# Optimization experiments

Measured on AMD Instinct MI355X. Metric: run time of the kernel, lower is better.

The kernel has to match this reference:

```python
import jax, jax.numpy as jnp
import numpy as np

WINDOW = 1024
UNITS = 128


def setup_inputs() -> dict:
    key = jax.random.key(0)
    k1, k2, k3 = jax.random.split(key, 3)
    input_tensor = jax.random.normal(k1, (1, UNITS), dtype=jnp.float32)
    state = jax.random.normal(k2, (UNITS, WINDOW), dtype=jnp.float32)
    w = jax.random.normal(k3, (2 * UNITS + 1, UNITS), dtype=jnp.float32) * 0.05
    b = jnp.zeros((UNITS,), dtype=jnp.float32)
    return {"input_tensor": input_tensor, "state": state, "w": w, "b": b}


def reference(input_tensor, state, w, b):
    U, W = state.shape
    # state @ state_shift (shift matrix with ones on subdiagonal) == drop first column
    shifted_state = state[:, 1:]                          # [U, W-1]
    new_state = jnp.concatenate([shifted_state, input_tensor.T], axis=-1)  # [U, W]
    fs = new_state.T                                      # flip_state: [W, U]

    # h_i[i,j,:] = fs[j];  h_j[i,j,:] = fs[i]
    # se_ij = concat([h_i, h_j, <h_i,h_j>], -1); sim = se_ij @ w + b
    # Split w so we never materialize the [W,W,2U+1] concat tensor:
    w_hi = w[:U]        # [U, U] multiplies h_i (fs[j])
    w_hj = w[U:2 * U]   # [U, U] multiplies h_j (fs[i])
    w_dot = w[2 * U]    # [U]    multiplies the pairwise dot product

    proj_hi = fs @ w_hi                                   # [W, U], indexed by j
    proj_hj = fs @ w_hj                                   # [W, U], indexed by i
    d = fs @ fs.T                                         # [W, W] pairwise dots

    # sim[i,j,u] = proj_hi[j,u] + proj_hj[i,u] + d[i,j]*w_dot[u] + b[u]
    sim = proj_hi[None, :, :] + proj_hj[:, None, :] + d[:, :, None] * w_dot + b  # [W,W,U]
    a = jax.nn.softmax(sim, axis=1)                       # softmax over j

    # c[i,u] = sum_j h_i[i,j,u] * a[i,j,u] = sum_j fs[j,u] * a[i,j,u]
    c = jnp.einsum('ju,iju->iu', fs, a)                   # [W, U]
    c_last = c[-1].reshape(1, U)                          # [1, U]
    return c_last
```

## Files before the change

### kernel.cpp

```cpp
#include <hip/hip_runtime.h>


constexpr int U    = 128;
constexpr int W    = 1024;
constexpr int JT   = 16;
constexpr int SSTR = 132;

__global__ __launch_bounds__(256) void rsa_part(
    const float* __restrict__ input,
    const float* __restrict__ state,
    const float* __restrict__ w,
    float* __restrict__ ws)
{
    const int bid = blockIdx.x;
    const int jt  = bid >> 2;
    const int uq  = bid & 3;
    const int t   = threadIdx.x;
    const int uu  = t & 7;
    const int j   = (t >> 3) & 15;
    const int kh  = t >> 7;

    __shared__ __align__(16) float sliceT[JT][SSTR];
    __shared__ __align__(16) float vv[U][32];
    __shared__ __align__(16) float sin_[U];
    __shared__ __align__(16) float mrg[JT][8][4];
    __shared__ __align__(16) float red2[2][8][8];

    float4 in4;
    if (t < 32) in4 = ((const float4*)input)[t];
    const float4 wdq = ((const float4*)(w + 2 * U * U + uq * 32))[uu];
    float4 wh[4];
    #pragma unroll
    for (int i = 0; i < 4; ++i) {
        const int k = (t >> 3) + 32 * i;
        wh[i] = ((const float4*)w)[k * 32 + uq * 8 + uu];
    }
    float4 st[2];
    #pragma unroll
    for (int i = 0; i < 2; ++i) {
        const int p = t + 256 * i;
        const int k = p >> 2;
        const int j4 = p & 3;
        st[i] = ((const float4*)state)[k * 256 + jt * 4 + j4];
    }

    if (t < 32) ((float4*)sin_)[t] = in4;
    __syncthreads();

    #pragma unroll
    for (int i = 0; i < 4; ++i) {
        const int k = (t >> 3) + 32 * i;
        const float ik = sin_[k];
        float4 r;
        r.x = fmaf(wdq.x, ik, wh[i].x);
        r.y = fmaf(wdq.y, ik, wh[i].y);
        r.z = fmaf(wdq.z, ik, wh[i].z);
        r.w = fmaf(wdq.w, ik, wh[i].w);
        *(float4*)&vv[k][4 * uu] = r;
    }
    #pragma unroll
    for (int i = 0; i < 2; ++i) {
        const int p = t + 256 * i;
        const int k = p >> 2;
        const int j4 = p & 3;
        sliceT[4 * j4 + 0][k] = st[i].x;
        sliceT[4 * j4 + 1][k] = st[i].y;
        sliceT[4 * j4 + 2][k] = st[i].z;
        sliceT[4 * j4 + 3][k] = st[i].w;
    }
    __syncthreads();
    if (jt == 0 && t < U) sliceT[0][t] = sin_[t];
    __syncthreads();

    const int kb0 = kh * 64;
    const float* aR = &sliceT[j][kb0];
    float4 acc = {0.f, 0.f, 0.f, 0.f};
    #pragma unroll
    for (int kc = 0; kc < 16; ++kc) {
        const float4 a4 = *(const float4*)(aR + 4 * kc);
        const float4 v0 = *(const float4*)&vv[kb0 + 4 * kc + 0][4 * uu];
        const float4 v1 = *(const float4*)&vv[kb0 + 4 * kc + 1][4 * uu];
        const float4 v2 = *(const float4*)&vv[kb0 + 4 * kc + 2][4 * uu];
        const float4 v3 = *(const float4*)&vv[kb0 + 4 * kc + 3][4 * uu];
        acc.x = fmaf(a4.x, v0.x, acc.x); acc.y = fmaf(a4.x, v0.y, acc.y);
        acc.z = fmaf(a4.x, v0.z, acc.z); acc.w = fmaf(a4.x, v0.w, acc.w);
        acc.x = fmaf(a4.y, v1.x, acc.x); acc.y = fmaf(a4.y, v1.y, acc.y);
        acc.z = fmaf(a4.y, v1.z, acc.z); acc.w = fmaf(a4.y, v1.w, acc.w);
        acc.x = fmaf(a4.z, v2.x, acc.x); acc.y = fmaf(a4.z, v2.y, acc.y);
        acc.z = fmaf(a4.z, v2.z, acc.z); acc.w = fmaf(a4.z, v2.w, acc.w);
        acc.x = fmaf(a4.w, v3.x, acc.x); acc.y = fmaf(a4.w, v3.y, acc.y);
        acc.z = fmaf(a4.w, v3.z, acc.z); acc.w = fmaf(a4.w, v3.w, acc.w);
    }

    if (kh) *(float4*)&mrg[j][uu][0] = acc;
    __syncthreads();
    if (!kh) {
        const float4 o = *(const float4*)&mrg[j][uu][0];
        acc.x += o.x; acc.y += o.y; acc.z += o.z; acc.w += o.w;

        const float4 fs4 = *(const float4*)&sliceT[j][uq * 32 + 4 * uu];
        float4 e, n;
        e.x = __expf(acc.x); e.y = __expf(acc.y);
        e.z = __expf(acc.z); e.w = __expf(acc.w);
        n.x = fs4.x * e.x;   n.y = fs4.y * e.y;
        n.z = fs4.z * e.z;   n.w = fs4.w * e.w;

        #pragma unroll
        for (int o8 = 8; o8 < 64; o8 <<= 1) {
            n.x += __shfl_down(n.x, o8, 64); n.y += __shfl_down(n.y, o8, 64);
            n.z += __shfl_down(n.z, o8, 64); n.w += __shfl_down(n.w, o8, 64);
            e.x += __shfl_down(e.x, o8, 64); e.y += __shfl_down(e.y, o8, 64);
            e.z += __shfl_down(e.z, o8, 64); e.w += __shfl_down(e.w, o8, 64);
        }
        const int lane = t & 63, wv = t >> 6;
        if (lane < 8) {
            red2[wv][lane][0] = n.x; red2[wv][lane][1] = n.y;
            red2[wv][lane][2] = n.z; red2[wv][lane][3] = n.w;
            red2[wv][lane][4] = e.x; red2[wv][lane][5] = e.y;
            red2[wv][lane][6] = e.z; red2[wv][lane][7] = e.w;
        }
    }
    __syncthreads();

    if (t < 32) {
        const int ug = t >> 2, m = t & 3;
        const float num = red2[0][ug][m]     + red2[1][ug][m];
        const float den = red2[0][ug][4 + m] + red2[1][ug][4 + m];
        const int base = (uq * 64 + jt) * 64;
        ws[base + t]      = num;
        ws[base + 32 + t] = den;
    }
}

__global__ __launch_bounds__(256) void rsa_fin(
    const float* __restrict__ ws, float* __restrict__ out)
{
    __shared__ float sden[U];
    const int t  = threadIdx.x;
    const int u  = t & (U - 1);
    const int nd = t >> 7;
    const float* base = ws + (size_t)(u >> 5) * 64 * 64 + nd * 32 + (u & 31);
    float s = 0.0f;
    #pragma unroll 16
    for (int jt = 0; jt < 64; ++jt) s += base[jt * 64];
    if (nd) sden[u] = s;
    __syncthreads();
    if (!nd) out[u] = s / sden[u];
}

extern "C" void kernel_launch(void* const* d_in, const int* in_sizes, int n_in,
                              void* d_out, int out_size, void* d_ws, size_t ws_size,
                              hipStream_t stream) {
    const float* input = (const float*)d_in[0];
    const float* state = (const float*)d_in[1];
    const float* w     = (const float*)d_in[2];
    float* out = (float*)d_out;
    float* ws  = (float*)d_ws;

    rsa_part<<<dim3(256), dim3(256), 0, stream>>>(input, state, w, ws);
    rsa_fin<<<dim3(1), dim3(256), 0, stream>>>(ws, out);
}
```

Measured before the change: 62.55 us.

## Fuse partial and final reduction into one per-unit softmax kernel

Replaces the two-kernel scheme (tiled partial sums written to workspace, then a single-block final reduction) with one kernel that launches a block per output unit. Each thread computes logits for four window columns with a k-loop that streams state rows through an 8-deep register prefetch ring. The block then reduces numerator and denominator in-block and writes the result directly. This removes the second launch and the workspace round-trip, but every block now rereads the whole state matrix from cache and the k-loop is a long chain of dependent loads.

```diff
diff --git a/kernel.cpp b/kernel.cpp
--- a/kernel.cpp
+++ b/kernel.cpp
@@ -1,151 +1,77 @@
 #include <hip/hip_runtime.h>
 
 
-constexpr int U    = 128;
-constexpr int W    = 1024;
-constexpr int JT   = 16;
-constexpr int SSTR = 132;
+constexpr int U = 128;
+constexpr int W = 1024;
 
-__global__ __launch_bounds__(256) void rsa_part(
+__global__ __launch_bounds__(256) void rsa_fused(
     const float* __restrict__ input,
     const float* __restrict__ state,
     const float* __restrict__ w,
-    float* __restrict__ ws)
+    float* __restrict__ out)
 {
-    const int bid = blockIdx.x;
-    const int jt  = bid >> 2;
-    const int uq  = bid & 3;
-    const int t   = threadIdx.x;
-    const int uu  = t & 7;
-    const int j   = (t >> 3) & 15;
-    const int kh  = t >> 7;
+    const int u = blockIdx.x;
+    const int t = threadIdx.x;
 
-    __shared__ __align__(16) float sliceT[JT][SSTR];
-    __shared__ __align__(16) float vv[U][32];
-    __shared__ __align__(16) float sin_[U];
-    __shared__ __align__(16) float mrg[JT][8][4];
-    __shared__ __align__(16) float red2[2][8][8];
+    __shared__ __align__(8) float kdat[U][2];
+    __shared__ float red[4][2];
 
-    float4 in4;
-    if (t < 32) in4 = ((const float4*)input)[t];
-    const float4 wdq = ((const float4*)(w + 2 * U * U + uq * 32))[uu];
-    float4 wh[4];
+    const float* sp = state + 4 * t;
+    constexpr int PF = 8;
+    float4 pf[PF];
     #pragma unroll
-    for (int i = 0; i < 4; ++i) {
-        const int k = (t >> 3) + 32 * i;
-        wh[i] = ((const float4*)w)[k * 32 + uq * 8 + uu];
-    }
-    float4 st[2];
-    #pragma unroll
-    for (int i = 0; i < 2; ++i) {
-        const int p = t + 256 * i;
-        const int k = p >> 2;
-        const int j4 = p & 3;
-        st[i] = ((const float4*)state)[k * 256 + jt * 4 + j4];
+    for (int i = 0; i < PF; ++i)
+        pf[i] = *(const float4*)(sp + i * W);
+
+    float4 nw = *(const float4*)(state + (size_t)u * W + 4 * t);
+    const float in_u = input[u];
+
+    float vk = 0.f, ik = 0.f;
+    if (t < U) {
+        const float whi = w[t * U + u];
+        ik = input[t];
+        const float wd = w[2 * U * U + u];
+        vk = fmaf(wd, ik, whi);
     }
 
-    if (t < 32) ((float4*)sin_)[t] = in4;
+    if (t < U) { kdat[t][0] = vk; kdat[t][1] = ik; }
     __syncthreads();
 
-    #pragma unroll
-    for (int i = 0; i < 4; ++i) {
-        const int k = (t >> 3) + 32 * i;
-        const float ik = sin_[k];
-        float4 r;
-        r.x = fmaf(wdq.x, ik, wh[i].x);
-        r.y = fmaf(wdq.y, ik, wh[i].y);
-        r.z = fmaf(wdq.z, ik, wh[i].z);
-        r.w = fmaf(wdq.w, ik, wh[i].w);
-        *(float4*)&vv[k][4 * uu] = r;
-    }
-    #pragma unroll
-    for (int i = 0; i < 2; ++i) {
-        const int p = t + 256 * i;
-        const int k = p >> 2;
-        const int j4 = p & 3;
-        sliceT[4 * j4 + 0][k] = st[i].x;
-        sliceT[4 * j4 + 1][k] = st[i].y;
-        sliceT[4 * j4 + 2][k] = st[i].z;
-        sliceT[4 * j4 + 3][k] = st[i].w;
-    }
-    __syncthreads();
-    if (jt == 0 && t < U) sliceT[0][t] = sin_[t];
-    __syncthreads();
-
-    const int kb0 = kh * 64;
-    const float* aR = &sliceT[j][kb0];
+    const bool t0 = (t == 0);
     float4 acc = {0.f, 0.f, 0.f, 0.f};
     #pragma unroll
-    for (int kc = 0; kc < 16; ++kc) {
-        const float4 a4 = *(const float4*)(aR + 4 * kc);
-        const float4 v0 = *(const float4*)&vv[kb0 + 4 * kc + 0][4 * uu];
-        const float4 v1 = *(const float4*)&vv[kb0 + 4 * kc + 1][4 * uu];
-        const float4 v2 = *(const float4*)&vv[kb0 + 4 * kc + 2][4 * uu];
-        const float4 v3 = *(const float4*)&vv[kb0 + 4 * kc + 3][4 * uu];
-        acc.x = fmaf(a4.x, v0.x, acc.x); acc.y = fmaf(a4.x, v0.y, acc.y);
-        acc.z = fmaf(a4.x, v0.z, acc.z); acc.w = fmaf(a4.x, v0.w, acc.w);
-        acc.x = fmaf(a4.y, v1.x, acc.x); acc.y = fmaf(a4.y, v1.y, acc.y);
-        acc.z = fmaf(a4.y, v1.z, acc.z); acc.w = fmaf(a4.y, v1.w, acc.w);
-        acc.x = fmaf(a4.z, v2.x, acc.x); acc.y = fmaf(a4.z, v2.y, acc.y);
-        acc.z = fmaf(a4.z, v2.z, acc.z); acc.w = fmaf(a4.z, v2.w, acc.w);
-        acc.x = fmaf(a4.w, v3.x, acc.x); acc.y = fmaf(a4.w, v3.y, acc.y);
-        acc.z = fmaf(a4.w, v3.z, acc.z); acc.w = fmaf(a4.w, v3.w, acc.w);
+    for (int k = 0; k < U; ++k) {
+        float4 cur = pf[k & (PF - 1)];
+        if (k + PF < U)
+            pf[k & (PF - 1)] = *(const float4*)(sp + (k + PF) * W);
+        const float2 kd = *(const float2*)&kdat[k][0];
+        const float fs0 = t0 ? kd.y : cur.x;
+        acc.x = fmaf(fs0,   kd.x, acc.x);
+        acc.y = fmaf(cur.y, kd.x, acc.y);
+        acc.z = fmaf(cur.z, kd.x, acc.z);
+        acc.w = fmaf(cur.w, kd.x, acc.w);
     }
 
-    if (kh) *(float4*)&mrg[j][uu][0] = acc;
+    if (t0) nw.x = in_u;
+    float4 e;
+    e.x = __expf(acc.x); e.y = __expf(acc.y);
+    e.z = __expf(acc.z); e.w = __expf(acc.w);
+    float num = nw.x * e.x + nw.y * e.y + nw.z * e.z + nw.w * e.w;
+    float den = e.x + e.y + e.z + e.w;
+
+    #pragma unroll
+    for (int o = 32; o >= 1; o >>= 1) {
+        num += __shfl_down(num, o, 64);
+        den += __shfl_down(den, o, 64);
+    }
+    const int lane = t & 63, wv = t >> 6;
+    if (lane == 0) { red[wv][0] = num; red[wv][1] = den; }
     __syncthreads();
-    if (!kh) {
-        const float4 o = *(const float4*)&mrg[j][uu][0];
-        acc.x += o.x; acc.y += o.y; acc.z += o.z; acc.w += o.w;
-
-        const float4 fs4 = *(const float4*)&sliceT[j][uq * 32 + 4 * uu];
-        float4 e, n;
-        e.x = __expf(acc.x); e.y = __expf(acc.y);
-        e.z = __expf(acc.z); e.w = __expf(acc.w);
-        n.x = fs4.x * e.x;   n.y = fs4.y * e.y;
-        n.z = fs4.z * e.z;   n.w = fs4.w * e.w;
-
-        #pragma unroll
-        for (int o8 = 8; o8 < 64; o8 <<= 1) {
-            n.x += __shfl_down(n.x, o8, 64); n.y += __shfl_down(n.y, o8, 64);
-            n.z += __shfl_down(n.z, o8, 64); n.w += __shfl_down(n.w, o8, 64);
-            e.x += __shfl_down(e.x, o8, 64); e.y += __shfl_down(e.y, o8, 64);
-            e.z += __shfl_down(e.z, o8, 64); e.w += __shfl_down(e.w, o8, 64);
-        }
-        const int lane = t & 63, wv = t >> 6;
-        if (lane < 8) {
-            red2[wv][lane][0] = n.x; red2[wv][lane][1] = n.y;
-            red2[wv][lane][2] = n.z; red2[wv][lane][3] = n.w;
-            red2[wv][lane][4] = e.x; red2[wv][lane][5] = e.y;
-            red2[wv][lane][6] = e.z; red2[wv][lane][7] = e.w;
-        }
+    if (t0) {
+        const float n = red[0][0] + red[1][0] + red[2][0] + red[3][0];
+        const float d = red[0][1] + red[1][1] + red[2][1] + red[3][1];
+        out[u] = n / d;
     }
-    __syncthreads();
-
-    if (t < 32) {
-        const int ug = t >> 2, m = t & 3;
-        const float num = red2[0][ug][m]     + red2[1][ug][m];
-        const float den = red2[0][ug][4 + m] + red2[1][ug][4 + m];
-        const int base = (uq * 64 + jt) * 64;
-        ws[base + t]      = num;
-        ws[base + 32 + t] = den;
-    }
-}
-
-__global__ __launch_bounds__(256) void rsa_fin(
-    const float* __restrict__ ws, float* __restrict__ out)
-{
-    __shared__ float sden[U];
-    const int t  = threadIdx.x;
-    const int u  = t & (U - 1);
-    const int nd = t >> 7;
-    const float* base = ws + (size_t)(u >> 5) * 64 * 64 + nd * 32 + (u & 31);
-    float s = 0.0f;
-    #pragma unroll 16
-    for (int jt = 0; jt < 64; ++jt) s += base[jt * 64];
-    if (nd) sden[u] = s;
-    __syncthreads();
-    if (!nd) out[u] = s / sden[u];
 }
 
 extern "C" void kernel_launch(void* const* d_in, const int* in_sizes, int n_in,
@@ -155,8 +81,6 @@
     const float* state = (const float*)d_in[1];
     const float* w     = (const float*)d_in[2];
     float* out = (float*)d_out;
-    float* ws  = (float*)d_ws;
 
-    rsa_part<<<dim3(256), dim3(256), 0, stream>>>(input, state, w, ws);
-    rsa_fin<<<dim3(1), dim3(256), 0, stream>>>(ws, out);
+    rsa_fused<<<dim3(128), dim3(256), 0, stream>>>(input, state, w, out);
 }
```

Result: slower. 64.88 us (+3.7%).
